# Kernel tuning notes

Measured on AMD Instinct MI355X. Metric: run time of the kernel, lower is better.

The kernel has to match this reference:

```python
import jax, jax.numpy as jnp
import numpy as np

D_MODEL = 512
N_EXPERTS = 8


def setup_inputs() -> dict:
    key = jax.random.key(0)
    ks = jax.random.split(key, 7)
    B, S, D, E = 8, 2048, D_MODEL, N_EXPERTS
    scale = 1.0 / np.sqrt(D)
    x = jax.random.normal(ks[0], (B, S, D), dtype=jnp.float32)
    W1 = jax.random.normal(ks[1], (E, D, D), dtype=jnp.float32) * scale
    b1 = jax.random.normal(ks[2], (E, D), dtype=jnp.float32) * scale
    W2 = jax.random.normal(ks[3], (E, D, D), dtype=jnp.float32) * scale
    b2 = jax.random.normal(ks[4], (E, D), dtype=jnp.float32) * scale
    Wg = jax.random.normal(ks[5], (D, E), dtype=jnp.float32) * scale
    bg = jax.random.normal(ks[6], (E,), dtype=jnp.float32) * scale
    return {"x": x, "W1": W1, "b1": b1, "W2": W2, "b2": b2, "Wg": Wg, "bg": bg}


def reference(x, W1, b1, W2, b2, Wg, bg):
    # All-experts dense MLP: h[e,b,s,f] = relu(x @ W1[e] + b1[e])
    h = jax.nn.relu(jnp.einsum('bsd,edf->ebsf', x, W1) + b1[:, None, None, :])
    expert_out = jnp.einsum('ebsf,efd->ebsd', h, W2) + b2[:, None, None, :]
    # Softmax gate over experts
    gates = jax.nn.softmax(jnp.einsum('bsd,de->bse', x, Wg) + bg, axis=-1)
    # Weighted combine: bsn, nbsd -> bsd
    return jnp.einsum('bsn,nbsd->bsd', gates, expert_out)
```

## Files before the change

kernel.cpp:

```cpp
#include <hip/hip_runtime.h>

typedef __attribute__((ext_vector_type(8))) short short8;
typedef __attribute__((ext_vector_type(4))) float f32x4;
typedef __attribute__((ext_vector_type(16))) float f32x16;

#define T_TOK 16384
#define DM 512
#define NE 8
#define BM 64
#define ROWB 1040

__device__ __forceinline__ ushort f2bf(float v) {
  unsigned u = __float_as_uint(v);
  return (ushort)((u + 0x7FFFu + ((u >> 16) & 1u)) >> 16);
}

__device__ __forceinline__ unsigned pk2bf(float a, float b) {
  unsigned r;
  asm("v_cvt_pk_bf16_f32 %0, %1, %2" : "=v"(r) : "v"(a), "v"(b));
  return r;
}

__global__ void gates_kernel(const float* __restrict__ x, const float* __restrict__ Wg,
                             const float* __restrict__ bg, float* __restrict__ gates) {
  int wid = (int)((blockIdx.x * blockDim.x + threadIdx.x) >> 6);
  int lane = threadIdx.x & 63;
  if (wid >= T_TOK) return;
  const float* xt = x + (size_t)wid * DM;
  float a[NE];
#pragma unroll
  for (int e = 0; e < NE; ++e) a[e] = 0.f;
  for (int d = lane; d < DM; d += 64) {
    float xv = xt[d];
    const float* wr = Wg + d * NE;
#pragma unroll
    for (int e = 0; e < NE; ++e) a[e] += xv * wr[e];
  }
#pragma unroll
  for (int e = 0; e < NE; ++e) {
#pragma unroll
    for (int off = 32; off > 0; off >>= 1) a[e] += __shfl_xor(a[e], off, 64);
  }
  float m = -1e30f;
#pragma unroll
  for (int e = 0; e < NE; ++e) { a[e] += bg[e]; m = fmaxf(m, a[e]); }
  float s = 0.f;
#pragma unroll
  for (int e = 0; e < NE; ++e) { a[e] = __expf(a[e] - m); s += a[e]; }
  float inv = 1.f / s;
  if (lane < NE) gates[(size_t)wid * NE + lane] = a[lane] * inv;
}

__global__ void reorder_w_kernel(const float* __restrict__ W, ushort* __restrict__ WF) {
  int c = blockIdx.x * blockDim.x + threadIdx.x;
  int l = c & 63;
  int chunk = c >> 6;
  int ft = chunk & 15;
  int kh = (chunk >> 4) & 31;
  int e = chunk >> 9;
  int n = ft * 32 + (l & 31);
  int k0 = kh * 16 + (l >> 5) * 8;
  const float* src = W + ((size_t)e * DM + k0) * DM + n;
  short8 v;
#pragma unroll
  for (int j = 0; j < 8; ++j) v[j] = (short)f2bf(src[(size_t)j * DM]);
  *reinterpret_cast<short8*>(WF + (size_t)c * 8) = v;
}

__global__ __launch_bounds__(512, 2) void moe_main_kernel(
    const float* __restrict__ x, const ushort* __restrict__ W1F,
    const float* __restrict__ b1, const ushort* __restrict__ W2F,
    const float* __restrict__ b2, const float* __restrict__ gates,
    float* __restrict__ out) {
  extern __shared__ char smem[];
  char* x_lds = smem;
  char* h_lds = smem + 66560;
  float* g_lds = (float*)(smem + 133120);

  const int tid = threadIdx.x;
  const int lane = tid & 63;
  const int w = tid >> 6;
  const int hi = lane >> 5;
  const int l31 = lane & 31;
  const int m0 = blockIdx.x * BM;

  const unsigned abase = (unsigned)l31 * ROWB + (unsigned)hi * 16;
  const unsigned wbase = (unsigned)l31 * ROWB + (unsigned)(w * 128 + hi * 8);

#define BARRIER()                                        \
  do {                                                   \
    asm volatile("s_waitcnt lgkmcnt(0)" ::: "memory");   \
    __builtin_amdgcn_s_barrier();                        \
  } while (0)

#define LDACT(lds, kt, ks, ni) \
  (*reinterpret_cast<const short8*>((lds) + abase + (ni) * (32 * ROWB) + ((kt) * 64 + (ks) * 32)))

#define MF(d, a, b) d = __builtin_amdgcn_mfma_f32_32x32x16_bf16(a, b, d, 0, 0, 0)

  {
    int t = tid >> 3, e = tid & 7;
    g_lds[t * 9 + e] = gates[(size_t)(m0 + t) * NE + e];
  }

  for (int i = tid; i < BM * DM / 4; i += 512) {
    int t = i >> 7;
    int kd = (i & 127) * 4;
    float4 v = *reinterpret_cast<const float4*>(x + ((size_t)(m0 + t) << 9) + kd);
    unsigned lo = pk2bf(v.x, v.y);
    unsigned hb = pk2bf(v.z, v.w);
    *reinterpret_cast<uint2*>(x_lds + (unsigned)(t * ROWB + kd * 2)) = make_uint2(lo, hb);
  }
  BARRIER();

  const short8* wp1 = reinterpret_cast<const short8*>(W1F) + w * 128 + lane;
  const short8* wp2 = reinterpret_cast<const short8*>(W2F) + w * 128 + lane;

  f32x16 acc[2][2];
#pragma unroll
  for (int mi = 0; mi < 2; ++mi)
#pragma unroll
    for (int ni = 0; ni < 2; ++ni)
#pragma unroll
      for (int i = 0; i < 16; ++i) acc[mi][ni][i] = 0.f;

  short8 wb[3][4], ab[2][4];

#pragma unroll
  for (int ks = 0; ks < 2; ++ks)
#pragma unroll
    for (int mi = 0; mi < 2; ++mi) {
      wb[2][ks * 2 + mi] = wp1[ks * 1024 + mi * 64];
      wb[0][ks * 2 + mi] = wp1[2048 + ks * 1024 + mi * 64];
    }
#pragma unroll
  for (int ks = 0; ks < 2; ++ks)
#pragma unroll
    for (int ni = 0; ni < 2; ++ni) ab[0][ks * 2 + ni] = LDACT(x_lds, 0, ks, ni);

  for (int e = 0; e < NE; ++e) {
    const short8* we1 = wp1 + (size_t)e * 32768;
    const short8* we2 = wp2 + (size_t)e * 32768;

    f32x16 hacc[2][2];
#pragma unroll
    for (int mi = 0; mi < 2; ++mi)
#pragma unroll
      for (int ni = 0; ni < 2; ++ni)
#pragma unroll
        for (int i = 0; i < 16; ++i) hacc[mi][ni][i] = 0.f;

#pragma unroll
    for (int kt = 0; kt < 16; ++kt) {
      if (kt < 14) {
#pragma unroll
        for (int ks = 0; ks < 2; ++ks)
#pragma unroll
          for (int mi = 0; mi < 2; ++mi)
            wb[(kt + 1) % 3][ks * 2 + mi] = we1[(kt + 2) * 2048 + ks * 1024 + mi * 64];
      }
      if (kt < 15) {
#pragma unroll
        for (int ks = 0; ks < 2; ++ks)
#pragma unroll
          for (int ni = 0; ni < 2; ++ni)
            ab[(kt + 1) % 2][ks * 2 + ni] = LDACT(x_lds, kt + 1, ks, ni);
      }
      __builtin_amdgcn_s_setprio(1);
#pragma unroll
      for (int ks = 0; ks < 2; ++ks)
#pragma unroll
        for (int mi = 0; mi < 2; ++mi)
#pragma unroll
          for (int ni = 0; ni < 2; ++ni)
            MF(hacc[mi][ni], wb[(kt + 2) % 3][ks * 2 + mi], ab[kt % 2][ks * 2 + ni]);
      __builtin_amdgcn_s_setprio(0);
    }

#pragma unroll
    for (int ks = 0; ks < 2; ++ks)
#pragma unroll
      for (int mi = 0; mi < 2; ++mi) {
        wb[1][ks * 2 + mi] = we2[ks * 1024 + mi * 64];
        wb[2][ks * 2 + mi] = we2[2048 + ks * 1024 + mi * 64];
      }

#pragma unroll
    for (int ni = 0; ni < 2; ++ni) {
      int t = ni * 32 + l31;
      float g = g_lds[t * 9 + e];
#pragma unroll
      for (int mi = 0; mi < 2; ++mi) {
#pragma unroll
        for (int j = 0; j < 4; ++j) {
          float4 b1q = *reinterpret_cast<const float4*>(
              b1 + e * DM + w * 64 + mi * 32 + j * 8 + hi * 4);
          float v0 = fmaxf(hacc[mi][ni][j * 4 + 0] + b1q.x, 0.f) * g;
          float v1 = fmaxf(hacc[mi][ni][j * 4 + 1] + b1q.y, 0.f) * g;
          float v2 = fmaxf(hacc[mi][ni][j * 4 + 2] + b1q.z, 0.f) * g;
          float v3 = fmaxf(hacc[mi][ni][j * 4 + 3] + b1q.w, 0.f) * g;
          unsigned lo = pk2bf(v0, v1);
          unsigned hb = pk2bf(v2, v3);
          *reinterpret_cast<uint2*>(h_lds + wbase + ni * (32 * ROWB) + mi * 64 + j * 16) =
              make_uint2(lo, hb);
        }
      }
    }
    BARRIER();

#pragma unroll
    for (int ks = 0; ks < 2; ++ks)
#pragma unroll
      for (int ni = 0; ni < 2; ++ni) ab[0][ks * 2 + ni] = LDACT(h_lds, 0, ks, ni);

#pragma unroll
    for (int kt = 0; kt < 16; ++kt) {
      if (kt < 14) {
#pragma unroll
        for (int ks = 0; ks < 2; ++ks)
#pragma unroll
          for (int mi = 0; mi < 2; ++mi)
            wb[kt % 3][ks * 2 + mi] = we2[(kt + 2) * 2048 + ks * 1024 + mi * 64];
      }
      if (kt < 15) {
#pragma unroll
        for (int ks = 0; ks < 2; ++ks)
#pragma unroll
          for (int ni = 0; ni < 2; ++ni)
            ab[(kt + 1) % 2][ks * 2 + ni] = LDACT(h_lds, kt + 1, ks, ni);
      }
      __builtin_amdgcn_s_setprio(1);
#pragma unroll
      for (int ks = 0; ks < 2; ++ks)
#pragma unroll
        for (int mi = 0; mi < 2; ++mi)
#pragma unroll
          for (int ni = 0; ni < 2; ++ni)
            MF(acc[mi][ni], wb[(kt + 1) % 3][ks * 2 + mi], ab[kt % 2][ks * 2 + ni]);
      __builtin_amdgcn_s_setprio(0);
    }

    if (e < NE - 1) {
      const short8* wn1 = we1 + 32768;
#pragma unroll
      for (int ks = 0; ks < 2; ++ks)
#pragma unroll
        for (int mi = 0; mi < 2; ++mi) {
          wb[2][ks * 2 + mi] = wn1[ks * 1024 + mi * 64];
          wb[0][ks * 2 + mi] = wn1[2048 + ks * 1024 + mi * 64];
        }
#pragma unroll
      for (int ks = 0; ks < 2; ++ks)
#pragma unroll
        for (int ni = 0; ni < 2; ++ni) ab[0][ks * 2 + ni] = LDACT(x_lds, 0, ks, ni);
    }
    BARRIER();
  }

#pragma unroll
  for (int e = 0; e < NE; ++e) {
    float ge0 = g_lds[l31 * 9 + e];
    float ge1 = g_lds[(32 + l31) * 9 + e];
#pragma unroll
    for (int mi = 0; mi < 2; ++mi)
#pragma unroll
      for (int j = 0; j < 4; ++j) {
        float4 b2q = *reinterpret_cast<const float4*>(
            b2 + e * DM + w * 64 + mi * 32 + j * 8 + hi * 4);
        acc[mi][0][j * 4 + 0] += ge0 * b2q.x;
        acc[mi][0][j * 4 + 1] += ge0 * b2q.y;
        acc[mi][0][j * 4 + 2] += ge0 * b2q.z;
        acc[mi][0][j * 4 + 3] += ge0 * b2q.w;
        acc[mi][1][j * 4 + 0] += ge1 * b2q.x;
        acc[mi][1][j * 4 + 1] += ge1 * b2q.y;
        acc[mi][1][j * 4 + 2] += ge1 * b2q.z;
        acc[mi][1][j * 4 + 3] += ge1 * b2q.w;
      }
  }

#pragma unroll
  for (int ni = 0; ni < 2; ++ni) {
    int t = m0 + ni * 32 + l31;
#pragma unroll
    for (int mi = 0; mi < 2; ++mi)
#pragma unroll
      for (int j = 0; j < 4; ++j) {
        f32x4 v;
        v[0] = acc[mi][ni][j * 4 + 0];
        v[1] = acc[mi][ni][j * 4 + 1];
        v[2] = acc[mi][ni][j * 4 + 2];
        v[3] = acc[mi][ni][j * 4 + 3];
        *reinterpret_cast<f32x4*>(out + (size_t)t * DM + w * 64 + mi * 32 + j * 8 + hi * 4) = v;
      }
  }
#undef LDACT
#undef MF
#undef BARRIER
}

extern "C" void kernel_launch(void* const* d_in, const int* in_sizes, int n_in,
                              void* d_out, int out_size, void* d_ws, size_t ws_size,
                              hipStream_t stream) {
  const float* x  = (const float*)d_in[0];
  const float* W1 = (const float*)d_in[1];
  const float* b1 = (const float*)d_in[2];
  const float* W2 = (const float*)d_in[3];
  const float* b2 = (const float*)d_in[4];
  const float* Wg = (const float*)d_in[5];
  const float* bg = (const float*)d_in[6];
  float* out = (float*)d_out;

  float* gates = (float*)d_ws;
  ushort* W1F = (ushort*)((char*)d_ws + 524288);
  ushort* W2F = (ushort*)((char*)d_ws + 524288 + 4194304);

  hipFuncSetAttribute((const void*)moe_main_kernel,
                      hipFuncAttributeMaxDynamicSharedMemorySize, 135424);

  gates_kernel<<<T_TOK / 4, 256, 0, stream>>>(x, Wg, bg, gates);
  reorder_w_kernel<<<1024, 256, 0, stream>>>(W1, W1F);
  reorder_w_kernel<<<1024, 256, 0, stream>>>(W2, W2F);
  moe_main_kernel<<<T_TOK / BM, 512, 135424, stream>>>(x, W1F, b1, W2F, b2, gates, out);
}
```

Before: 163.4 us.

## Double-buffer hidden activations and stream pre-laid-out bf16 x from global

Result: slower. 250.0 us (+53.0%).

```diff
diff --git a/kernel.cpp b/kernel.cpp
--- a/kernel.cpp
+++ b/kernel.cpp
@@ -20,6 +20,8 @@
   asm("v_cvt_pk_bf16_f32 %0, %1, %2" : "=v"(r) : "v"(a), "v"(b));
   return r;
 }
+
+#define MF(d, a, b) d = __builtin_amdgcn_mfma_f32_32x32x16_bf16(a, b, d, 0, 0, 0)
 
 __global__ void gates_kernel(const float* __restrict__ x, const float* __restrict__ Wg,
                              const float* __restrict__ bg, float* __restrict__ gates) {
@@ -67,15 +69,114 @@
   *reinterpret_cast<short8*>(WF + (size_t)c * 8) = v;
 }
 
+__global__ void reorder_x_kernel(const float* __restrict__ x, ushort* __restrict__ XF) {
+  int c = blockIdx.x * blockDim.x + threadIdx.x;
+  int l = c & 63;
+  int ni = (c >> 6) & 1;
+  int ks = (c >> 7) & 1;
+  int kt = (c >> 8) & 15;
+  int m = c >> 12;
+  int t = m * 64 + ni * 32 + (l & 31);
+  int k0 = kt * 32 + ks * 16 + (l >> 5) * 8;
+  const float* src = x + (size_t)t * DM + k0;
+  short8 v;
+#pragma unroll
+  for (int j = 0; j < 8; ++j) v[j] = (short)f2bf(src[j]);
+  *reinterpret_cast<short8*>(XF + (size_t)c * 8) = v;
+}
+
+__device__ __forceinline__ void g1_gemm(const short8* __restrict__ wp,
+                                        const short8* __restrict__ xfp,
+                                        short8 (&wb)[3][4], short8 (&ab)[2][4],
+                                        f32x16 (&hacc)[2][2]) {
+#pragma unroll
+  for (int ks = 0; ks < 2; ++ks)
+#pragma unroll
+    for (int mi = 0; mi < 2; ++mi) {
+      wb[2][ks * 2 + mi] = wp[ks * 1024 + mi * 64];
+      wb[0][ks * 2 + mi] = wp[2048 + ks * 1024 + mi * 64];
+    }
+#pragma unroll
+  for (int ks = 0; ks < 2; ++ks)
+#pragma unroll
+    for (int ni = 0; ni < 2; ++ni) ab[0][ks * 2 + ni] = xfp[(ks * 2 + ni) * 64];
+#pragma unroll
+  for (int kt = 0; kt < 16; ++kt) {
+    if (kt < 14) {
+#pragma unroll
+      for (int ks = 0; ks < 2; ++ks)
+#pragma unroll
+        for (int mi = 0; mi < 2; ++mi)
+          wb[(kt + 1) % 3][ks * 2 + mi] = wp[(kt + 2) * 2048 + ks * 1024 + mi * 64];
+    }
+    if (kt < 15) {
+#pragma unroll
+      for (int ks = 0; ks < 2; ++ks)
+#pragma unroll
+        for (int ni = 0; ni < 2; ++ni)
+          ab[(kt + 1) & 1][ks * 2 + ni] = xfp[((kt + 1) * 4 + ks * 2 + ni) * 64];
+    }
+    __builtin_amdgcn_s_setprio(1);
+#pragma unroll
+    for (int ks = 0; ks < 2; ++ks)
+#pragma unroll
+      for (int mi = 0; mi < 2; ++mi)
+#pragma unroll
+        for (int ni = 0; ni < 2; ++ni)
+          MF(hacc[mi][ni], wb[(kt + 2) % 3][ks * 2 + mi], ab[kt % 2][ks * 2 + ni]);
+    __builtin_amdgcn_s_setprio(0);
+  }
+}
+
+__device__ __forceinline__ void g2_gemm(const short8* __restrict__ we2,
+                                        const char* __restrict__ hsrc, unsigned abase,
+                                        short8 (&wb)[3][4], short8 (&ab)[2][4],
+                                        f32x16 (&acc)[2][2]) {
+#pragma unroll
+  for (int ks = 0; ks < 2; ++ks)
+#pragma unroll
+    for (int ni = 0; ni < 2; ++ni)
+      ab[0][ks * 2 + ni] = *reinterpret_cast<const short8*>(
+          hsrc + abase + ni * (32 * ROWB) + ks * 32);
+#pragma unroll
+  for (int kt = 0; kt < 16; ++kt) {
+    if (kt < 14) {
+#pragma unroll
+      for (int ks = 0; ks < 2; ++ks)
+#pragma unroll
+        for (int mi = 0; mi < 2; ++mi)
+          wb[kt % 3][ks * 2 + mi] = we2[(kt + 2) * 2048 + ks * 1024 + mi * 64];
+    }
+    if (kt < 15) {
+#pragma unroll
+      for (int ks = 0; ks < 2; ++ks)
+#pragma unroll
+        for (int ni = 0; ni < 2; ++ni)
+          ab[(kt + 1) & 1][ks * 2 + ni] = *reinterpret_cast<const short8*>(
+              hsrc + abase + ni * (32 * ROWB) + (kt + 1) * 64 + ks * 32);
+    }
+    __builtin_amdgcn_s_setprio(1);
+#pragma unroll
+    for (int ks = 0; ks < 2; ++ks)
+#pragma unroll
+      for (int mi = 0; mi < 2; ++mi)
+#pragma unroll
+        for (int ni = 0; ni < 2; ++ni)
+          MF(acc[mi][ni], wb[(kt + 1) % 3][ks * 2 + mi], ab[kt % 2][ks * 2 + ni]);
+    __builtin_amdgcn_s_setprio(0);
+  }
+}
+
 __global__ __launch_bounds__(512, 2) void moe_main_kernel(
-    const float* __restrict__ x, const ushort* __restrict__ W1F,
+    const ushort* __restrict__ XF, const ushort* __restrict__ W1F,
     const float* __restrict__ b1, const ushort* __restrict__ W2F,
     const float* __restrict__ b2, const float* __restrict__ gates,
     float* __restrict__ out) {
   extern __shared__ char smem[];
-  char* x_lds = smem;
-  char* h_lds = smem + 66560;
+  char* hb0 = smem;
+  char* hb1 = smem + 66560;
   float* g_lds = (float*)(smem + 133120);
+  float* b1_lds = (float*)(smem + 135424);
 
   const int tid = threadIdx.x;
   const int lane = tid & 63;
@@ -93,168 +194,110 @@
     __builtin_amdgcn_s_barrier();                        \
   } while (0)
 
-#define LDACT(lds, kt, ks, ni) \
-  (*reinterpret_cast<const short8*>((lds) + abase + (ni) * (32 * ROWB) + ((kt) * 64 + (ks) * 32)))
-
-#define MF(d, a, b) d = __builtin_amdgcn_mfma_f32_32x32x16_bf16(a, b, d, 0, 0, 0)
-
   {
     int t = tid >> 3, e = tid & 7;
     g_lds[t * 9 + e] = gates[(size_t)(m0 + t) * NE + e];
   }
-
-  for (int i = tid; i < BM * DM / 4; i += 512) {
-    int t = i >> 7;
-    int kd = (i & 127) * 4;
-    float4 v = *reinterpret_cast<const float4*>(x + ((size_t)(m0 + t) << 9) + kd);
-    unsigned lo = pk2bf(v.x, v.y);
-    unsigned hb = pk2bf(v.z, v.w);
-    *reinterpret_cast<uint2*>(x_lds + (unsigned)(t * ROWB + kd * 2)) = make_uint2(lo, hb);
-  }
-  BARRIER();
+  {
+    float4* dst = (float4*)b1_lds;
+    const float4* src = (const float4*)b1;
+    dst[tid] = src[tid];
+    dst[tid + 512] = src[tid + 512];
+  }
 
   const short8* wp1 = reinterpret_cast<const short8*>(W1F) + w * 128 + lane;
   const short8* wp2 = reinterpret_cast<const short8*>(W2F) + w * 128 + lane;
-
-  f32x16 acc[2][2];
+  const short8* xfp = reinterpret_cast<const short8*>(XF) + (size_t)blockIdx.x * 4096 + lane;
+
+  f32x16 acc[2][2], hacc[2][2];
 #pragma unroll
   for (int mi = 0; mi < 2; ++mi)
 #pragma unroll
     for (int ni = 0; ni < 2; ++ni)
 #pragma unroll
-      for (int i = 0; i < 16; ++i) acc[mi][ni][i] = 0.f;
+      for (int i = 0; i < 16; ++i) { acc[mi][ni][i] = 0.f; hacc[mi][ni][i] = 0.f; }
 
   short8 wb[3][4], ab[2][4];
 
+  BARRIER();
+
+  g1_gemm(wp1, xfp, wb, ab, hacc);
+
 #pragma unroll
   for (int ks = 0; ks < 2; ++ks)
 #pragma unroll
     for (int mi = 0; mi < 2; ++mi) {
-      wb[2][ks * 2 + mi] = wp1[ks * 1024 + mi * 64];
-      wb[0][ks * 2 + mi] = wp1[2048 + ks * 1024 + mi * 64];
-    }
-#pragma unroll
-  for (int ks = 0; ks < 2; ++ks)
-#pragma unroll
-    for (int ni = 0; ni < 2; ++ni) ab[0][ks * 2 + ni] = LDACT(x_lds, 0, ks, ni);
+      wb[1][ks * 2 + mi] = wp2[ks * 1024 + mi * 64];
+      wb[2][ks * 2 + mi] = wp2[2048 + ks * 1024 + mi * 64];
+    }
+
+#pragma unroll
+  for (int ni = 0; ni < 2; ++ni) {
+    int t = ni * 32 + l31;
+    float g = g_lds[t * 9 + 0];
+#pragma unroll
+    for (int mi = 0; mi < 2; ++mi) {
+#pragma unroll
+      for (int j = 0; j < 4; ++j) {
+        float4 b1q = *reinterpret_cast<const float4*>(
+            b1_lds + 0 * DM + w * 64 + mi * 32 + j * 8 + hi * 4);
+        float v0 = fmaxf(hacc[mi][ni][j * 4 + 0] + b1q.x, 0.f) * g;
+        float v1 = fmaxf(hacc[mi][ni][j * 4 + 1] + b1q.y, 0.f) * g;
+        float v2 = fmaxf(hacc[mi][ni][j * 4 + 2] + b1q.z, 0.f) * g;
+        float v3 = fmaxf(hacc[mi][ni][j * 4 + 3] + b1q.w, 0.f) * g;
+        *reinterpret_cast<uint2*>(hb0 + wbase + ni * (32 * ROWB) + mi * 64 + j * 16) =
+            make_uint2(pk2bf(v0, v1), pk2bf(v2, v3));
+      }
+    }
+  }
+  BARRIER();
 
   for (int e = 0; e < NE; ++e) {
-    const short8* we1 = wp1 + (size_t)e * 32768;
     const short8* we2 = wp2 + (size_t)e * 32768;
-
-    f32x16 hacc[2][2];
-#pragma unroll
-    for (int mi = 0; mi < 2; ++mi)
-#pragma unroll
-      for (int ni = 0; ni < 2; ++ni)
-#pragma unroll
-        for (int i = 0; i < 16; ++i) hacc[mi][ni][i] = 0.f;
-
-#pragma unroll
-    for (int kt = 0; kt < 16; ++kt) {
-      if (kt < 14) {
-#pragma unroll
-        for (int ks = 0; ks < 2; ++ks)
-#pragma unroll
-          for (int mi = 0; mi < 2; ++mi)
-            wb[(kt + 1) % 3][ks * 2 + mi] = we1[(kt + 2) * 2048 + ks * 1024 + mi * 64];
-      }
-      if (kt < 15) {
-#pragma unroll
-        for (int ks = 0; ks < 2; ++ks)
-#pragma unroll
-          for (int ni = 0; ni < 2; ++ni)
-            ab[(kt + 1) % 2][ks * 2 + ni] = LDACT(x_lds, kt + 1, ks, ni);
-      }
-      __builtin_amdgcn_s_setprio(1);
-#pragma unroll
-      for (int ks = 0; ks < 2; ++ks)
-#pragma unroll
-        for (int mi = 0; mi < 2; ++mi)
-#pragma unroll
-          for (int ni = 0; ni < 2; ++ni)
-            MF(hacc[mi][ni], wb[(kt + 2) % 3][ks * 2 + mi], ab[kt % 2][ks * 2 + ni]);
-      __builtin_amdgcn_s_setprio(0);
-    }
-
-#pragma unroll
-    for (int ks = 0; ks < 2; ++ks)
-#pragma unroll
-      for (int mi = 0; mi < 2; ++mi) {
-        wb[1][ks * 2 + mi] = we2[ks * 1024 + mi * 64];
-        wb[2][ks * 2 + mi] = we2[2048 + ks * 1024 + mi * 64];
-      }
-
-#pragma unroll
-    for (int ni = 0; ni < 2; ++ni) {
-      int t = ni * 32 + l31;
-      float g = g_lds[t * 9 + e];
-#pragma unroll
-      for (int mi = 0; mi < 2; ++mi) {
-#pragma unroll
-        for (int j = 0; j < 4; ++j) {
-          float4 b1q = *reinterpret_cast<const float4*>(
-              b1 + e * DM + w * 64 + mi * 32 + j * 8 + hi * 4);
-          float v0 = fmaxf(hacc[mi][ni][j * 4 + 0] + b1q.x, 0.f) * g;
-          float v1 = fmaxf(hacc[mi][ni][j * 4 + 1] + b1q.y, 0.f) * g;
-          float v2 = fmaxf(hacc[mi][ni][j * 4 + 2] + b1q.z, 0.f) * g;
-          float v3 = fmaxf(hacc[mi][ni][j * 4 + 3] + b1q.w, 0.f) * g;
-          unsigned lo = pk2bf(v0, v1);
-          unsigned hb = pk2bf(v2, v3);
-          *reinterpret_cast<uint2*>(h_lds + wbase + ni * (32 * ROWB) + mi * 64 + j * 16) =
-              make_uint2(lo, hb);
+    char* hsrc = (e & 1) ? hb1 : hb0;
+
+    g2_gemm(we2, hsrc, abase, wb, ab, acc);
+
+    if (e < NE - 1) {
+#pragma unroll
+      for (int mi = 0; mi < 2; ++mi)
+#pragma unroll
+        for (int ni = 0; ni < 2; ++ni)
+#pragma unroll
+          for (int i = 0; i < 16; ++i) hacc[mi][ni][i] = 0.f;
+      g1_gemm(wp1 + (size_t)(e + 1) * 32768, xfp, wb, ab, hacc);
+
+      const short8* wn2 = we2 + 32768;
+#pragma unroll
+      for (int ks = 0; ks < 2; ++ks)
+#pragma unroll
+        for (int mi = 0; mi < 2; ++mi) {
+          wb[1][ks * 2 + mi] = wn2[ks * 1024 + mi * 64];
+          wb[2][ks * 2 + mi] = wn2[2048 + ks * 1024 + mi * 64];
+        }
+
+      char* hdst = ((e + 1) & 1) ? hb1 : hb0;
+#pragma unroll
+      for (int ni = 0; ni < 2; ++ni) {
+        int t = ni * 32 + l31;
+        float g = g_lds[t * 9 + (e + 1)];
+#pragma unroll
+        for (int mi = 0; mi < 2; ++mi) {
+#pragma unroll
+          for (int j = 0; j < 4; ++j) {
+            float4 b1q = *reinterpret_cast<const float4*>(
+                b1_lds + (e + 1) * DM + w * 64 + mi * 32 + j * 8 + hi * 4);
+            float v0 = fmaxf(hacc[mi][ni][j * 4 + 0] + b1q.x, 0.f) * g;
+            float v1 = fmaxf(hacc[mi][ni][j * 4 + 1] + b1q.y, 0.f) * g;
+            float v2 = fmaxf(hacc[mi][ni][j * 4 + 2] + b1q.z, 0.f) * g;
+            float v3 = fmaxf(hacc[mi][ni][j * 4 + 3] + b1q.w, 0.f) * g;
+            *reinterpret_cast<uint2*>(hdst + wbase + ni * (32 * ROWB) + mi * 64 + j * 16) =
+                make_uint2(pk2bf(v0, v1), pk2bf(v2, v3));
+          }
         }
       }
-    }
-    BARRIER();
-
-#pragma unroll
-    for (int ks = 0; ks < 2; ++ks)
-#pragma unroll
-      for (int ni = 0; ni < 2; ++ni) ab[0][ks * 2 + ni] = LDACT(h_lds, 0, ks, ni);
-
-#pragma unroll
-    for (int kt = 0; kt < 16; ++kt) {
-      if (kt < 14) {
-#pragma unroll
-        for (int ks = 0; ks < 2; ++ks)
-#pragma unroll
-          for (int mi = 0; mi < 2; ++mi)
-            wb[kt % 3][ks * 2 + mi] = we2[(kt + 2) * 2048 + ks * 1024 + mi * 64];
-      }
-      if (kt < 15) {
-#pragma unroll
-        for (int ks = 0; ks < 2; ++ks)
-#pragma unroll
-          for (int ni = 0; ni < 2; ++ni)
-            ab[(kt + 1) % 2][ks * 2 + ni] = LDACT(h_lds, kt + 1, ks, ni);
-      }
-      __builtin_amdgcn_s_setprio(1);
-#pragma unroll
-      for (int ks = 0; ks < 2; ++ks)
-#pragma unroll
-        for (int mi = 0; mi < 2; ++mi)
-#pragma unroll
-          for (int ni = 0; ni < 2; ++ni)
-            MF(acc[mi][ni], wb[(kt + 1) % 3][ks * 2 + mi], ab[kt % 2][ks * 2 + ni]);
-      __builtin_amdgcn_s_setprio(0);
-    }
-
-    if (e < NE - 1) {
-      const short8* wn1 = we1 + 32768;
-#pragma unroll
-      for (int ks = 0; ks < 2; ++ks)
-#pragma unroll
-        for (int mi = 0; mi < 2; ++mi) {
-          wb[2][ks * 2 + mi] = wn1[ks * 1024 + mi * 64];
-          wb[0][ks * 2 + mi] = wn1[2048 + ks * 1024 + mi * 64];
-        }
-#pragma unroll
-      for (int ks = 0; ks < 2; ++ks)
-#pragma unroll
-        for (int ni = 0; ni < 2; ++ni) ab[0][ks * 2 + ni] = LDACT(x_lds, 0, ks, ni);
-    }
-    BARRIER();
+      BARRIER();
+    }
   }
 
 #pragma unroll
@@ -293,8 +336,6 @@
         *reinterpret_cast<f32x4*>(out + (size_t)t * DM + w * 64 + mi * 32 + j * 8 + hi * 4) = v;
       }
   }
-#undef LDACT
-#undef MF
 #undef BARRIER
 }
 
@@ -312,13 +353,15 @@
 
   float* gates = (float*)d_ws;
   ushort* W1F = (ushort*)((char*)d_ws + 524288);
-  ushort* W2F = (ushort*)((char*)d_ws + 524288 + 4194304);
+  ushort* W2F = (ushort*)((char*)d_ws + 4718592);
+  ushort* XF  = (ushort*)((char*)d_ws + 8912896);
 
   hipFuncSetAttribute((const void*)moe_main_kernel,
-                      hipFuncAttributeMaxDynamicSharedMemorySize, 135424);
+                      hipFuncAttributeMaxDynamicSharedMemorySize, 151808);
 
   gates_kernel<<<T_TOK / 4, 256, 0, stream>>>(x, Wg, bg, gates);
   reorder_w_kernel<<<1024, 256, 0, stream>>>(W1, W1F);
   reorder_w_kernel<<<1024, 256, 0, stream>>>(W2, W2F);
-  moe_main_kernel<<<T_TOK / BM, 512, 135424, stream>>>(x, W1F, b1, W2F, b2, gates, out);
-}
+  reorder_x_kernel<<<4096, 256, 0, stream>>>(x, XF);
+  moe_main_kernel<<<T_TOK / BM, 512, 151808, stream>>>(XF, W1F, b1, W2F, b2, gates, out);
+}
```

## Fuse gate softmax into main MoE kernel and merge weight reorder launches

Applied to the files above, without the earlier changes.

Measured after the change: 155.4 us. 4.9% less time.

```diff
diff --git a/kernel.cpp b/kernel.cpp
--- a/kernel.cpp
+++ b/kernel.cpp
@@ -21,38 +21,15 @@
   return r;
 }
 
-__global__ void gates_kernel(const float* __restrict__ x, const float* __restrict__ Wg,
-                             const float* __restrict__ bg, float* __restrict__ gates) {
-  int wid = (int)((blockIdx.x * blockDim.x + threadIdx.x) >> 6);
-  int lane = threadIdx.x & 63;
-  if (wid >= T_TOK) return;
-  const float* xt = x + (size_t)wid * DM;
-  float a[NE];
-#pragma unroll
-  for (int e = 0; e < NE; ++e) a[e] = 0.f;
-  for (int d = lane; d < DM; d += 64) {
-    float xv = xt[d];
-    const float* wr = Wg + d * NE;
-#pragma unroll
-    for (int e = 0; e < NE; ++e) a[e] += xv * wr[e];
-  }
-#pragma unroll
-  for (int e = 0; e < NE; ++e) {
-#pragma unroll
-    for (int off = 32; off > 0; off >>= 1) a[e] += __shfl_xor(a[e], off, 64);
-  }
-  float m = -1e30f;
-#pragma unroll
-  for (int e = 0; e < NE; ++e) { a[e] += bg[e]; m = fmaxf(m, a[e]); }
-  float s = 0.f;
-#pragma unroll
-  for (int e = 0; e < NE; ++e) { a[e] = __expf(a[e] - m); s += a[e]; }
-  float inv = 1.f / s;
-  if (lane < NE) gates[(size_t)wid * NE + lane] = a[lane] * inv;
-}
-
-__global__ void reorder_w_kernel(const float* __restrict__ W, ushort* __restrict__ WF) {
+#define MF(d, a, b) d = __builtin_amdgcn_mfma_f32_32x32x16_bf16(a, b, d, 0, 0, 0)
+
+__global__ void reorder_w_kernel(const float* __restrict__ W1, const float* __restrict__ W2,
+                                 ushort* __restrict__ W1F, ushort* __restrict__ W2F) {
   int c = blockIdx.x * blockDim.x + threadIdx.x;
+  int which = c >> 18;
+  c &= (1 << 18) - 1;
+  const float* W = which ? W2 : W1;
+  ushort* WF = which ? W2F : W1F;
   int l = c & 63;
   int chunk = c >> 6;
   int ft = chunk & 15;
@@ -70,12 +47,13 @@
 __global__ __launch_bounds__(512, 2) void moe_main_kernel(
     const float* __restrict__ x, const ushort* __restrict__ W1F,
     const float* __restrict__ b1, const ushort* __restrict__ W2F,
-    const float* __restrict__ b2, const float* __restrict__ gates,
-    float* __restrict__ out) {
+    const float* __restrict__ b2, const float* __restrict__ Wg,
+    const float* __restrict__ bg, float* __restrict__ out) {
   extern __shared__ char smem[];
   char* x_lds = smem;
   char* h_lds = smem + 66560;
   float* g_lds = (float*)(smem + 133120);
+  float* wg_lds = (float*)(smem + 135424);
 
   const int tid = threadIdx.x;
   const int lane = tid & 63;
@@ -96,20 +74,21 @@
 #define LDACT(lds, kt, ks, ni) \
   (*reinterpret_cast<const short8*>((lds) + abase + (ni) * (32 * ROWB) + ((kt) * 64 + (ks) * 32)))
 
-#define MF(d, a, b) d = __builtin_amdgcn_mfma_f32_32x32x16_bf16(a, b, d, 0, 0, 0)
+  const float bgv = bg[tid & 7];
 
   {
-    int t = tid >> 3, e = tid & 7;
-    g_lds[t * 9 + e] = gates[(size_t)(m0 + t) * NE + e];
+    float4* dst = (float4*)wg_lds;
+    const float4* src = (const float4*)Wg;
+    dst[tid] = src[tid];
+    dst[tid + 512] = src[tid + 512];
   }
 
   for (int i = tid; i < BM * DM / 4; i += 512) {
     int t = i >> 7;
     int kd = (i & 127) * 4;
     float4 v = *reinterpret_cast<const float4*>(x + ((size_t)(m0 + t) << 9) + kd);
-    unsigned lo = pk2bf(v.x, v.y);
-    unsigned hb = pk2bf(v.z, v.w);
-    *reinterpret_cast<uint2*>(x_lds + (unsigned)(t * ROWB + kd * 2)) = make_uint2(lo, hb);
+    *reinterpret_cast<uint2*>(x_lds + (unsigned)(t * ROWB + kd * 2)) =
+        make_uint2(pk2bf(v.x, v.y), pk2bf(v.z, v.w));
   }
   BARRIER();
 
@@ -137,6 +116,32 @@
   for (int ks = 0; ks < 2; ++ks)
 #pragma unroll
     for (int ni = 0; ni < 2; ++ni) ab[0][ks * 2 + ni] = LDACT(x_lds, 0, ks, ni);
+
+  {
+    int t = tid >> 3, e = tid & 7;
+    const char* xrow = x_lds + (unsigned)(t * ROWB);
+    float lg = 0.f;
+    for (int d0 = 0; d0 < DM; d0 += 8) {
+      short8 xv = *reinterpret_cast<const short8*>(xrow + d0 * 2);
+#pragma unroll
+      for (int j = 0; j < 8; ++j) {
+        float xf = __uint_as_float(((unsigned)(ushort)xv[j]) << 16);
+        lg += xf * wg_lds[(d0 + j) * 8 + e];
+      }
+    }
+    lg += bgv;
+    float m = lg;
+    m = fmaxf(m, __shfl_xor(m, 1, 8));
+    m = fmaxf(m, __shfl_xor(m, 2, 8));
+    m = fmaxf(m, __shfl_xor(m, 4, 8));
+    float ex = __expf(lg - m);
+    float s = ex;
+    s += __shfl_xor(s, 1, 8);
+    s += __shfl_xor(s, 2, 8);
+    s += __shfl_xor(s, 4, 8);
+    g_lds[t * 9 + e] = ex / s;
+  }
+  BARRIER();
 
   for (int e = 0; e < NE; ++e) {
     const short8* we1 = wp1 + (size_t)e * 32768;
@@ -199,10 +204,8 @@
           float v1 = fmaxf(hacc[mi][ni][j * 4 + 1] + b1q.y, 0.f) * g;
           float v2 = fmaxf(hacc[mi][ni][j * 4 + 2] + b1q.z, 0.f) * g;
           float v3 = fmaxf(hacc[mi][ni][j * 4 + 3] + b1q.w, 0.f) * g;
-          unsigned lo = pk2bf(v0, v1);
-          unsigned hb = pk2bf(v2, v3);
           *reinterpret_cast<uint2*>(h_lds + wbase + ni * (32 * ROWB) + mi * 64 + j * 16) =
-              make_uint2(lo, hb);
+              make_uint2(pk2bf(v0, v1), pk2bf(v2, v3));
         }
       }
     }
@@ -294,7 +297,6 @@
       }
   }
 #undef LDACT
-#undef MF
 #undef BARRIER
 }
 
@@ -310,15 +312,12 @@
   const float* bg = (const float*)d_in[6];
   float* out = (float*)d_out;
 
-  float* gates = (float*)d_ws;
-  ushort* W1F = (ushort*)((char*)d_ws + 524288);
-  ushort* W2F = (ushort*)((char*)d_ws + 524288 + 4194304);
+  ushort* W1F = (ushort*)d_ws;
+  ushort* W2F = (ushort*)((char*)d_ws + 4194304);
 
   hipFuncSetAttribute((const void*)moe_main_kernel,
-                      hipFuncAttributeMaxDynamicSharedMemorySize, 135424);
-
-  gates_kernel<<<T_TOK / 4, 256, 0, stream>>>(x, Wg, bg, gates);
-  reorder_w_kernel<<<1024, 256, 0, stream>>>(W1, W1F);
-  reorder_w_kernel<<<1024, 256, 0, stream>>>(W2, W2F);
-  moe_main_kernel<<<T_TOK / BM, 512, 135424, stream>>>(x, W1F, b1, W2F, b2, gates, out);
-}
+                      hipFuncAttributeMaxDynamicSharedMemorySize, 151808);
+
+  reorder_w_kernel<<<2048, 256, 0, stream>>>(W1, W2, W1F, W2F);
+  moe_main_kernel<<<T_TOK / BM, 512, 151808, stream>>>(x, W1F, b1, W2F, b2, Wg, bg, out);
+}
```
